# Kernel optimization log

Hardware: AMD Instinct MI355X
Metric: run time of the kernel (lower is better)

Reference implementation:

```python
import jax, jax.numpy as jnp
import numpy as np

NEG = -1e30

def setup_inputs() -> dict:
    key = jax.random.key(0)
    ks = jax.random.split(key, 6)
    B, H, Lc, Lq = 32, 256, 1024, 256
    C = jax.random.normal(ks[0], (B, H, Lc), dtype=jnp.float32)
    Q = jax.random.normal(ks[1], (B, H, Lq), dtype=jnp.float32)
    cmask = jnp.ones((B, Lc), dtype=jnp.int32)
    qmask = jnp.ones((B, Lq), dtype=jnp.int32)
    # xavier_uniform on [3H,1]: bound = sqrt(6/(3H+1))
    bound = float(np.sqrt(6.0 / (3 * H + 1)))
    w = jax.random.uniform(ks[2], (3 * H,), minval=-bound, maxval=bound, dtype=jnp.float32)
    # kaiming_normal (relu, fan_in=4H): std = sqrt(2/(4H))
    W_res = jax.random.normal(ks[3], (H, 4 * H), dtype=jnp.float32) * float(np.sqrt(2.0 / (4 * H)))
    b_res = jnp.zeros((H,), dtype=jnp.float32)
    return {"C": C, "Q": Q, "cmask": cmask, "qmask": qmask, "w": w, "W_res": W_res, "b_res": b_res}

def reference(C, Q, cmask, qmask, w, W_res, b_res):
    H = w.shape[0] // 3
    Ct = jnp.transpose(C, (0, 2, 1))  # [B, Lc, H]
    Qt = jnp.transpose(Q, (0, 2, 1))  # [B, Lq, H]
    w1, w2, w3 = w[:H], w[H:2 * H], w[2 * H:]
    # trilinear similarity S[b,i,j] = Ct_i.w1 + Qt_j.w2 + (Ct_i*Qt_j).w3
    S = (jnp.einsum('blh,h->bl', Ct, w1)[:, :, None]
         + jnp.einsum('bmh,h->bm', Qt, w2)[:, None, :]
         + jnp.einsum('blh,bmh->blm', Ct * w3, Qt))  # [B, Lc, Lq]
    qm = qmask.astype(jnp.float32)[:, None, :]  # [B,1,Lq]
    cm = cmask.astype(jnp.float32)[:, :, None]  # [B,Lc,1]
    S_row = jax.nn.softmax(S + NEG * (1.0 - qm), axis=2)   # over questions
    S_col = jax.nn.softmax(S + NEG * (1.0 - cm), axis=1)   # over context
    A = jnp.einsum('blm,bmh->blh', S_row, Qt)  # [B, Lc, H]
    Bm = jnp.einsum('blm,bkm->blk', S_row, S_col)  # [B, Lc, Lc]
    Bv = jnp.einsum('blk,bkh->blh', Bm, Ct)  # [B, Lc, H]
    cat = jnp.concatenate([Ct, A, Ct * A, Ct * Bv], axis=2)  # [B, Lc, 4H]
    out = jax.nn.relu(jnp.einsum('blf,hf->blh', cat, W_res) + b_res)
    return jnp.transpose(out, (0, 2, 1))  # [B, H, Lc]
```

## Files before the change

### kernel.cpp

```cpp
#include <hip/hip_runtime.h>
#include <math.h>

#define NB 32
#define NH 256
#define NLC 1024
#define NLQ 256
#define NEGV (-1e30f)
#define TCH 8
#define KSPLIT 4

typedef short short8 __attribute__((ext_vector_type(8)));
typedef float f32x4 __attribute__((ext_vector_type(4)));

__device__ inline short bf16_of(float f) {
  union { float f; unsigned u; } v;
  v.f = f;
  unsigned r = (v.u + 0x7fffu + ((v.u >> 16) & 1u)) >> 16;
  return (short)r;
}
__device__ inline float f_of(short s) {
  union { unsigned u; float f; } v;
  v.u = ((unsigned)(unsigned short)s) << 16;
  return v.f;
}
__device__ inline short8 cvt8(float4 a, float4 b) {
  short8 o;
  o[0] = bf16_of(a.x); o[1] = bf16_of(a.y); o[2] = bf16_of(a.z); o[3] = bf16_of(a.w);
  o[4] = bf16_of(b.x); o[5] = bf16_of(b.y); o[6] = bf16_of(b.z); o[7] = bf16_of(b.w);
  return o;
}

#define XCD_SWZ(GX, GY, GZ, bx, by, bz)                                 \
  int bx, by, bz;                                                       \
  {                                                                     \
    int _lin = blockIdx.x + (GX) * (blockIdx.y + (GY) * blockIdx.z);    \
    const int _nwg = (GX) * (GY) * (GZ);                                \
    _lin = (_lin & 7) * (_nwg >> 3) + (_lin >> 3);                      \
    bx = _lin % (GX);                                                   \
    by = (_lin / (GX)) % (GY);                                          \
    bz = _lin / ((GX) * (GY));                                          \
  }

__device__ inline void lds_w8(short* lds, int r, int c, short8 v) {
  int byteoff = (r << 6) + (((c ^ ((r >> 1) & 3)) & 3) << 4);
  *(short8*)((char*)lds + byteoff) = v;
}
__device__ inline short8 lds_r8(const short* lds, int R, int g) {
  int byteoff = (R << 6) + (((g ^ ((R >> 1) & 3)) & 3) << 4);
  return *(const short8*)((const char*)lds + byteoff);
}
__device__ inline void stage_g(const short* src, int ld, short* lds, int t) {
  int L = t & 63, w = t >> 6;
  int cp = (L & 3) ^ ((L >> 3) & 3);
#pragma unroll
  for (int i = 0; i < 2; ++i) {
    int seg = w + i * 4;
    const short* g = src + (size_t)(seg * 16 + (L >> 2)) * ld + cp * 8;
    __builtin_amdgcn_global_load_lds(
        (const __attribute__((address_space(1))) unsigned int*)g,
        (__attribute__((address_space(3))) unsigned int*)(lds + seg * 512), 16,
        0, 0);
  }
}

#define GEMM_IDS                                       \
  int t = threadIdx.x, lane = t & 63, w = t >> 6;      \
  int ln = lane & 15, g = lane >> 4;                   \
  int wr = (w >> 1) << 6, wc = (w & 1) << 6;           \
  (void)wr; (void)wc;

#define MFMA_STEP(AS, BS)                                                      \
  {                                                                            \
    short8 af[4], bfr[4];                                                      \
    _Pragma("unroll") for (int mi = 0; mi < 4; ++mi) af[mi] =                  \
        lds_r8(AS, wr + mi * 16 + ln, g);                                      \
    _Pragma("unroll") for (int ni = 0; ni < 4; ++ni) bfr[ni] =                 \
        lds_r8(BS, wc + ni * 16 + ln, g);                                      \
    _Pragma("unroll") for (int mi = 0; mi < 4; ++mi)                           \
        _Pragma("unroll") for (int ni = 0; ni < 4; ++ni) acc[mi][ni] =         \
            __builtin_amdgcn_mfma_f32_16x16x32_bf16(af[mi], bfr[ni],           \
                                                    acc[mi][ni], 0, 0, 0);     \
  }

__global__ __launch_bounds__(256) void k_prep_c(const float* __restrict__ C,
                                                const float* __restrict__ w,
                                                short* __restrict__ Ct_lh,
                                                short* __restrict__ Cb_hl,
                                                float* __restrict__ s1p) {
  __shared__ float Ts[64][65];
  __shared__ float red[4][64];
  int b = blockIdx.z, h0 = blockIdx.y << 6, l0 = blockIdx.x << 6;
  int t = threadIdx.x;
  int hr = t >> 4, lc = (t & 15) << 2;
  const float* Cb = C + ((size_t)b * NH + h0) * NLC + l0;
#pragma unroll
  for (int i = 0; i < 4; ++i) {
    int h = hr + i * 16;
    float4 v = *(const float4*)&Cb[(size_t)h * NLC + lc];
    short4 cb;
    cb.x = bf16_of(v.x); cb.y = bf16_of(v.y);
    cb.z = bf16_of(v.z); cb.w = bf16_of(v.w);
    *(short4*)&Cb_hl[((size_t)b * NH + h0 + h) * NLC + l0 + lc] = cb;
    Ts[h][lc + 0] = v.x;
    Ts[h][lc + 1] = v.y;
    Ts[h][lc + 2] = v.z;
    Ts[h][lc + 3] = v.w;
  }
  __syncthreads();
  int lr = t >> 2, hc = (t & 3) << 4;
  short* dst = &Ct_lh[((size_t)b * NLC + l0 + lr) * NH + h0 + hc];
  short8 o0, o1;
#pragma unroll
  for (int j = 0; j < 8; ++j) o0[j] = bf16_of(Ts[hc + j][lr]);
#pragma unroll
  for (int j = 0; j < 8; ++j) o1[j] = bf16_of(Ts[hc + 8 + j][lr]);
  *(short8*)dst = o0;
  *(short8*)(dst + 8) = o1;
  int q = t >> 6, lq = t & 63;
  float a = 0.f;
#pragma unroll
  for (int j = 0; j < 16; ++j) a += Ts[(q << 4) + j][lq] * w[h0 + (q << 4) + j];
  red[q][lq] = a;
  __syncthreads();
  if (q == 0)
    s1p[((size_t)blockIdx.y * NB + b) * NLC + l0 + lq] =
        red[0][lq] + red[1][lq] + red[2][lq] + red[3][lq];
}

__global__ __launch_bounds__(256) void k_prep_q(const float* __restrict__ Q,
                                                const float* __restrict__ w,
                                                short* __restrict__ Qtw3,
                                                short* __restrict__ Qb_hm,
                                                float* __restrict__ s2p) {
  __shared__ float Ts[64][65];
  __shared__ float red[4][64];
  int b = blockIdx.z, h0 = blockIdx.y << 6, m0 = blockIdx.x << 6;
  int t = threadIdx.x;
  int hr = t >> 4, mc = (t & 15) << 2;
  const float* w3 = w + 2 * NH;
  const float* Qb = Q + ((size_t)b * NH + h0) * NLQ + m0;
#pragma unroll
  for (int i = 0; i < 4; ++i) {
    int h = hr + i * 16;
    float4 v = *(const float4*)&Qb[(size_t)h * NLQ + mc];
    short4 qb;
    qb.x = bf16_of(v.x); qb.y = bf16_of(v.y);
    qb.z = bf16_of(v.z); qb.w = bf16_of(v.w);
    *(short4*)&Qb_hm[((size_t)b * NH + h0 + h) * NLQ + m0 + mc] = qb;
    Ts[h][mc + 0] = v.x;
    Ts[h][mc + 1] = v.y;
    Ts[h][mc + 2] = v.z;
    Ts[h][mc + 3] = v.w;
  }
  __syncthreads();
  int mr = t >> 2, hc = (t & 3) << 4;
  short* dst = &Qtw3[((size_t)b * NLQ + m0 + mr) * NH + h0 + hc];
  short8 o0, o1;
#pragma unroll
  for (int j = 0; j < 8; ++j)
    o0[j] = bf16_of(Ts[hc + j][mr] * w3[h0 + hc + j]);
#pragma unroll
  for (int j = 0; j < 8; ++j)
    o1[j] = bf16_of(Ts[hc + 8 + j][mr] * w3[h0 + hc + 8 + j]);
  *(short8*)dst = o0;
  *(short8*)(dst + 8) = o1;
  int q = t >> 6, mq = t & 63;
  const float* w2 = w + NH;
  float a = 0.f;
#pragma unroll
  for (int j = 0; j < 16; ++j)
    a += Ts[(q << 4) + j][mq] * w2[h0 + (q << 4) + j];
  red[q][mq] = a;
  __syncthreads();
  if (q == 0)
    s2p[((size_t)blockIdx.y * NB + b) * NLQ + m0 + mq] =
        red[0][mq] + red[1][mq] + red[2][mq] + red[3][mq];
}

__global__ __launch_bounds__(256) void k_prep_bf16(const float* __restrict__ X,
                                                   short* __restrict__ Y) {
  size_t i = ((size_t)blockIdx.x * 256 + threadIdx.x) * 8;
  float4 v0 = *(const float4*)&X[i];
  float4 v1 = *(const float4*)&X[i + 4];
  *(short8*)&Y[i] = cvt8(v0, v1);
}

__global__ __launch_bounds__(256) void k_sgemm(
    const short* __restrict__ Ct_lh, const short* __restrict__ Qtw3,
    const float* __restrict__ s1p, const float* __restrict__ s2p,
    const int* __restrict__ cmask, float* __restrict__ S,
    float* __restrict__ pmax, float* __restrict__ psum) {
  __shared__ short As[2][4096], Bs[2][4096];
  __shared__ float cmsh[128];
  __shared__ float sredm[4][4][16], sreds[4][4][16];
  XCD_SWZ(NLQ / 128, NLC / 128, NB, bx, by, bz)
  int b = bz, l0 = by << 7, m0 = bx << 7;
  GEMM_IDS
  const short* Ag = Ct_lh + ((size_t)b * NLC + l0) * NH;
  const short* Bg = Qtw3 + ((size_t)b * NLQ + m0) * NH;
  f32x4 acc[4][4] = {};
  stage_g(Ag, NH, As[0], t);
  stage_g(Bg, NH, Bs[0], t);
  __syncthreads();
  int cur = 0;
  for (int kn = 32; kn <= NH; kn += 32) {
    if (kn < NH) {
      stage_g(Ag + kn, NH, As[cur ^ 1], t);
      stage_g(Bg + kn, NH, Bs[cur ^ 1], t);
    }
    MFMA_STEP(As[cur], Bs[cur])
    __syncthreads();
    cur ^= 1;
  }
  if (t < 128) cmsh[t] = cmask[b * NLC + l0 + t] ? 0.f : NEGV;
  __syncthreads();
  const int N1 = NB * NLC, N2 = NB * NLQ;
  float s1r[16], ncr[16];
#pragma unroll
  for (int mi = 0; mi < 4; ++mi)
#pragma unroll
    for (int r = 0; r < 4; ++r) {
      int lloc = wr + mi * 16 + g * 4 + r;
      int gl = b * NLC + l0 + lloc;
      s1r[mi * 4 + r] =
          s1p[gl] + s1p[N1 + gl] + s1p[2 * N1 + gl] + s1p[3 * N1 + gl];
      ncr[mi * 4 + r] = cmsh[lloc];
    }
  float s2v[4], mxc[4], smc[4];
#pragma unroll
  for (int ni = 0; ni < 4; ++ni) {
    int gm = b * NLQ + m0 + wc + ni * 16 + ln;
    s2v[ni] = s2p[gm] + s2p[N2 + gm] + s2p[2 * N2 + gm] + s2p[3 * N2 + gm];
    mxc[ni] = -INFINITY;
    smc[ni] = 0.f;
  }
#pragma unroll
  for (int ni = 0; ni < 4; ++ni)
#pragma unroll
    for (int mi = 0; mi < 4; ++mi)
#pragma unroll
      for (int r = 0; r < 4; ++r)
        mxc[ni] = fmaxf(mxc[ni],
                        acc[mi][ni][r] + s1r[mi * 4 + r] + s2v[ni] +
                            ncr[mi * 4 + r]);
#pragma unroll
  for (int ni = 0; ni < 4; ++ni) {
    int m = m0 + wc + ni * 16 + ln;
#pragma unroll
    for (int mi = 0; mi < 4; ++mi)
#pragma unroll
      for (int r = 0; r < 4; ++r) {
        int l = l0 + wr + mi * 16 + g * 4 + r;
        float sv = acc[mi][ni][r] + s1r[mi * 4 + r] + s2v[ni];
        S[((size_t)b * NLC + l) * NLQ + m] = sv;
        smc[ni] += expf(sv + ncr[mi * 4 + r] - mxc[ni]);
      }
  }
#pragma unroll
  for (int off = 16; off <= 32; off <<= 1)
#pragma unroll
    for (int ni = 0; ni < 4; ++ni) {
      float m2 = __shfl_xor(mxc[ni], off);
      float s2x = __shfl_xor(smc[ni], off);
      float nm = fmaxf(mxc[ni], m2);
      smc[ni] = smc[ni] * expf(mxc[ni] - nm) + s2x * expf(m2 - nm);
      mxc[ni] = nm;
    }
  if (lane < 16) {
#pragma unroll
    for (int ni = 0; ni < 4; ++ni) {
      sredm[w][ni][lane] = mxc[ni];
      sreds[w][ni][lane] = smc[ni];
    }
  }
  __syncthreads();
  if (t < 128) {
    int wcsel = t >> 6, nii = (t >> 4) & 3, lnn = t & 15;
    float mA = sredm[wcsel][nii][lnn], sA = sreds[wcsel][nii][lnn];
    float mB = sredm[wcsel + 2][nii][lnn], sB = sreds[wcsel + 2][nii][lnn];
    float nm = fmaxf(mA, mB);
    float sm = sA * expf(mA - nm) + sB * expf(mB - nm);
    int m = m0 + (wcsel << 6) + nii * 16 + lnn;
    size_t base = ((size_t)b * NLQ + m) * TCH + by;
    pmax[base] = nm;
    psum[base] = sm;
  }
}

__global__ __launch_bounds__(256) void k_colfin(const float* __restrict__ pmax,
                                                const float* __restrict__ psum,
                                                float* __restrict__ cmax,
                                                float* __restrict__ cinv) {
  int m = blockIdx.x * 256 + threadIdx.x;
  const float* pm = pmax + (size_t)m * TCH;
  const float* ps = psum + (size_t)m * TCH;
  float mx = pm[0], sm = ps[0];
#pragma unroll
  for (int c = 1; c < TCH; ++c) {
    float m2 = pm[c], s2 = ps[c];
    float nm = fmaxf(mx, m2);
    sm = sm * expf(mx - nm) + s2 * expf(m2 - nm);
    mx = nm;
  }
  cmax[m] = mx;
  cinv[m] = 1.0f / sm;
}

__global__ __launch_bounds__(256) void k_rowsoft(float* __restrict__ S,
                                                 const int* __restrict__ qmask,
                                                 const int* __restrict__ cmask,
                                                 const float* __restrict__ cmax,
                                                 const float* __restrict__ cinv) {
  int wave = threadIdx.x >> 6, lane = threadIdx.x & 63;
  int idx = (blockIdx.x << 2) + wave;
  int b = idx >> 10;
  float* row = S + (size_t)idx * NLQ;
  const int* qm = qmask + b * NLQ;
  int m4 = lane << 2;
  float4 v = *(const float4*)&row[m4];
  int4 q = *(const int4*)&qm[m4];
  float x0 = v.x + (q.x ? 0.f : NEGV);
  float x1 = v.y + (q.y ? 0.f : NEGV);
  float x2 = v.z + (q.z ? 0.f : NEGV);
  float x3 = v.w + (q.w ? 0.f : NEGV);
  float mx = fmaxf(fmaxf(x0, x1), fmaxf(x2, x3));
#pragma unroll
  for (int off = 32; off > 0; off >>= 1) mx = fmaxf(mx, __shfl_xor(mx, off));
  float p0 = expf(x0 - mx), p1 = expf(x1 - mx);
  float p2 = expf(x2 - mx), p3 = expf(x3 - mx);
  float sm = p0 + p1 + p2 + p3;
#pragma unroll
  for (int off = 32; off > 0; off >>= 1) sm += __shfl_xor(sm, off);
  float iv = 1.0f / sm;
  short4 o;
  o.x = bf16_of(p0 * iv);
  o.y = bf16_of(p1 * iv);
  o.z = bf16_of(p2 * iv);
  o.w = bf16_of(p3 * iv);
  float cmf = (float)cmask[idx];
  float4 cm4 = *(const float4*)&cmax[(b << 8) + m4];
  float4 ci4 = *(const float4*)&cinv[(b << 8) + m4];
  short4 oc;
  oc.x = bf16_of(expf(v.x - cm4.x) * ci4.x * cmf);
  oc.y = bf16_of(expf(v.y - cm4.y) * ci4.y * cmf);
  oc.z = bf16_of(expf(v.z - cm4.z) * ci4.z * cmf);
  oc.w = bf16_of(expf(v.w - cm4.w) * ci4.w * cmf);
  *(short4*)((short*)row + m4) = o;
  *(short4*)((short*)row + 256 + m4) = oc;
}

__global__ __launch_bounds__(256) void k_tgemm(const short* __restrict__ Cb_hl,
                                               const short* __restrict__ PcolS,
                                               float* __restrict__ Tp) {
  __shared__ short As[4096], Bs[4096];
  XCD_SWZ(4, KSPLIT, NB, bx, by, bz)
  int b = bz;
  int ks = by;
  int h0 = (bx & 1) << 7;
  int m0 = (bx >> 1) << 7;
  GEMM_IDS
  const short* Ag = Cb_hl + ((size_t)b * NH + h0) * NLC;
  const short* Pb = PcolS + (size_t)b * NLC * 512 + 256 + m0;
  f32x4 acc[4][4] = {};
  int kbeg = ks * (NLC / KSPLIT), kend = kbeg + NLC / KSPLIT;
  int lloc = t >> 3, g2 = lloc >> 3, kin = lloc & 7;
  int mbase = (t & 7) << 4;
  for (int k0 = kbeg; k0 < kend; k0 += 32) {
    __syncthreads();
    stage_g(Ag + k0, NLC, As, t);
    {
      const short* srow = Pb + (size_t)(k0 + lloc) * 512;
      short8 x0 = *(const short8*)&srow[mbase];
      short8 x1 = *(const short8*)&srow[mbase + 8];
#pragma unroll
      for (int j = 0; j < 8; ++j) {
        int R = mbase + j;
        int byteoff =
            (R << 6) + (((g2 ^ ((R >> 1) & 3)) & 3) << 4) + (kin << 1);
        *(short*)((char*)Bs + byteoff) = x0[j];
      }
#pragma unroll
      for (int j = 0; j < 8; ++j) {
        int R = mbase + 8 + j;
        int byteoff =
            (R << 6) + (((g2 ^ ((R >> 1) & 3)) & 3) << 4) + (kin << 1);
        *(short*)((char*)Bs + byteoff) = x1[j];
      }
    }
    __syncthreads();
    MFMA_STEP(As, Bs)
  }
  float* dst = Tp + ((size_t)ks * NB + b) * NH * NLQ;
#pragma unroll
  for (int mi = 0; mi < 4; ++mi)
#pragma unroll
    for (int ni = 0; ni < 4; ++ni)
#pragma unroll
      for (int r = 0; r < 4; ++r) {
        int h = h0 + wr + mi * 16 + g * 4 + r;
        int m = m0 + wc + ni * 16 + ln;
        dst[(size_t)h * NLQ + m] = acc[mi][ni][r];
      }
}

__global__ __launch_bounds__(256) void k_tfin(const float* __restrict__ Tp,
                                              short* __restrict__ Tt) {
  size_t i = ((size_t)blockIdx.x * 256 + threadIdx.x) * 4;
  const size_t stride = (size_t)NB * NH * NLQ;
  float4 s = *(const float4*)&Tp[i];
#pragma unroll
  for (int ks = 1; ks < KSPLIT; ++ks) {
    float4 v = *(const float4*)&Tp[i + ks * stride];
    s.x += v.x; s.y += v.y; s.z += v.z; s.w += v.w;
  }
  short4 o;
  o.x = bf16_of(s.x);
  o.y = bf16_of(s.y);
  o.z = bf16_of(s.z);
  o.w = bf16_of(s.w);
  *(short4*)&Tt[i] = o;
}

__global__ __launch_bounds__(256) void k_abgemm(
    const short* __restrict__ Prow, const short* __restrict__ Qb_hm,
    const short* __restrict__ Tt, const short* __restrict__ Ct_lh,
    short* __restrict__ A_lh, short* __restrict__ CtA_lh,
    short* __restrict__ CtBv_lh) {
  __shared__ short As[2][4096], Bs[2][4096];
  XCD_SWZ(4, NLC / 128, NB, bx, by, bz)
  int b = bz, l0 = by << 7, nb = bx;
  GEMM_IDS
  const short* Ag = Prow + ((size_t)b * NLC + l0) * 512;
  const short* Bbase = (nb < 2)
                           ? Qb_hm + ((size_t)b * NH + nb * 128) * NLQ
                           : Tt + ((size_t)b * NH + (nb - 2) * 128) * NLQ;
  f32x4 acc[4][4] = {};
  stage_g(Ag, 512, As[0], t);
  stage_g(Bbase, NLQ, Bs[0], t);
  __syncthreads();
  int cur = 0;
  for (int kn = 32; kn <= NLQ; kn += 32) {
    if (kn < NLQ) {
      stage_g(Ag + kn, 512, As[cur ^ 1], t);
      stage_g(Bbase + kn, NLQ, Bs[cur ^ 1], t);
    }
    MFMA_STEP(As[cur], Bs[cur])
    __syncthreads();
    cur ^= 1;
  }
  int hbase = (nb & 1) << 7;
  if (nb < 2) {
#pragma unroll
    for (int mi = 0; mi < 4; ++mi)
#pragma unroll
      for (int ni = 0; ni < 4; ++ni)
#pragma unroll
        for (int r = 0; r < 4; ++r) {
          int l = l0 + wr + mi * 16 + g * 4 + r;
          int h = hbase + wc + ni * 16 + ln;
          size_t off = ((size_t)b * NLC + l) * NH + h;
          float a = acc[mi][ni][r];
          A_lh[off] = bf16_of(a);
          CtA_lh[off] = bf16_of(f_of(Ct_lh[off]) * a);
        }
  } else {
#pragma unroll
    for (int mi = 0; mi < 4; ++mi)
#pragma unroll
      for (int ni = 0; ni < 4; ++ni)
#pragma unroll
        for (int r = 0; r < 4; ++r) {
          int l = l0 + wr + mi * 16 + g * 4 + r;
          int h = hbase + wc + ni * 16 + ln;
          size_t off = ((size_t)b * NLC + l) * NH + h;
          CtBv_lh[off] = bf16_of(f_of(Ct_lh[off]) * acc[mi][ni][r]);
        }
  }
}

__global__ __launch_bounds__(256) void k_out(
    const short* __restrict__ Wb, const short* __restrict__ Ct_lh,
    const short* __restrict__ A_lh, const short* __restrict__ CtA_lh,
    const short* __restrict__ CtBv_lh, const float* __restrict__ br,
    float* __restrict__ out) {
  __shared__ short As[2][4096], Bs[2][4096];
  XCD_SWZ(NLC / 128, NH / 128, NB, bx, by, bz)
  int b = bz, h0 = by << 7, l0 = bx << 7;
  GEMM_IDS
  const short* Wg = Wb + (size_t)h0 * (4 * NH);
  size_t boff = ((size_t)b * NLC + l0) * NH;
  f32x4 acc[4][4] = {};
  stage_g(Wg, 4 * NH, As[0], t);
  stage_g(Ct_lh + boff, NH, Bs[0], t);
  __syncthreads();
  int cur = 0;
  for (int kn = 32; kn <= 4 * NH; kn += 32) {
    bool has = kn < 4 * NH;
    if (has) {
      stage_g(Wg + kn, 4 * NH, As[cur ^ 1], t);
      int regn = kn >> 8, kon = kn & 255;
      const short* base = (regn == 0) ? Ct_lh
                          : (regn == 1) ? A_lh
                          : (regn == 2) ? CtA_lh : CtBv_lh;
      stage_g(base + boff + kon, NH, Bs[cur ^ 1], t);
    }
    MFMA_STEP(As[cur], Bs[cur])
    __syncthreads();
    cur ^= 1;
  }
#pragma unroll
  for (int mi = 0; mi < 4; ++mi)
#pragma unroll
    for (int ni = 0; ni < 4; ++ni) {
      int h = h0 + wr + mi * 16 + g * 4;
      int l = l0 + wc + ni * 16 + ln;
#pragma unroll
      for (int r = 0; r < 4; ++r) {
        float bias = br[h + r];
        out[((size_t)b * NH + h + r) * NLC + l] =
            fmaxf(acc[mi][ni][r] + bias, 0.f);
      }
    }
}

extern "C" void kernel_launch(void* const* d_in, const int* in_sizes, int n_in,
                              void* d_out, int out_size, void* d_ws,
                              size_t ws_size, hipStream_t stream) {
  (void)in_sizes;
  (void)n_in;
  (void)out_size;
  (void)ws_size;
  const float* C = (const float*)d_in[0];
  const float* Q = (const float*)d_in[1];
  const int* cmask = (const int*)d_in[2];
  const int* qmask = (const int*)d_in[3];
  const float* w = (const float*)d_in[4];
  const float* W = (const float*)d_in[5];
  const float* br = (const float*)d_in[6];
  float* out = (float*)d_out;

  char* p = (char*)d_ws;
  float* S = (float*)p;       p += (size_t)NB * NLC * NLQ * 4;
  short* Ct_lh = (short*)p;   p += (size_t)NB * NLC * NH * 2;
  short* A_lh = (short*)p;    p += (size_t)NB * NLC * NH * 2;
  short* CtBv_lh = (short*)p; p += (size_t)NB * NLC * NH * 2;
  short* CtA_lh = (short*)p;  p += (size_t)NB * NLC * NH * 2;
  short* Cb_hl = (short*)p;   p += (size_t)NB * NH * NLC * 2;
  short* Tt = (short*)p;      p += (size_t)NB * NH * NLQ * 2;
  short* Qtw3 = (short*)p;    p += (size_t)NB * NLQ * NH * 2;
  short* Qb_hm = (short*)p;   p += (size_t)NB * NH * NLQ * 2;
  short* Wb = (short*)p;      p += (size_t)NH * 4 * NH * 2;
  float* cmax = (float*)p;    p += (size_t)NB * NLQ * 4;
  float* cinv = (float*)p;    p += (size_t)NB * NLQ * 4;
  float* pmax = (float*)p;    p += (size_t)NB * NLQ * TCH * 4;
  float* psum = (float*)p;    p += (size_t)NB * NLQ * TCH * 4;
  float* s1p = (float*)p;     p += (size_t)4 * NB * NLC * 4;
  float* s2p = (float*)p;     p += (size_t)4 * NB * NLQ * 4;
  float* Tp = (float*)A_lh;
  short* Prow = (short*)S;

  k_prep_c<<<dim3(NLC / 64, NH / 64, NB), dim3(256), 0, stream>>>(C, w, Ct_lh,
                                                                  Cb_hl, s1p);
  k_prep_q<<<dim3(NLQ / 64, NH / 64, NB), dim3(256), 0, stream>>>(
      Q, w, Qtw3, Qb_hm, s2p);
  k_prep_bf16<<<dim3(NH * 4 * NH / 2048), dim3(256), 0, stream>>>(W, Wb);
  k_sgemm<<<dim3(NLQ / 128, NLC / 128, NB), dim3(256), 0, stream>>>(
      Ct_lh, Qtw3, s1p, s2p, cmask, S, pmax, psum);
  k_colfin<<<dim3(NB * NLQ / 256), dim3(256), 0, stream>>>(pmax, psum, cmax,
                                                           cinv);
  k_rowsoft<<<dim3(NB * NLC / 4), dim3(256), 0, stream>>>(S, qmask, cmask,
                                                          cmax, cinv);
  k_tgemm<<<dim3(4, KSPLIT, NB), dim3(256), 0, stream>>>(Cb_hl, Prow, Tp);
  k_tfin<<<dim3(NB * NH * NLQ / 1024), dim3(256), 0, stream>>>(Tp, Tt);
  k_abgemm<<<dim3(4, NLC / 128, NB), dim3(256), 0, stream>>>(
      Prow, Qb_hm, Tt, Ct_lh, A_lh, CtA_lh, CtBv_lh);
  k_out<<<dim3(NLC / 128, NH / 128, NB), dim3(256), 0, stream>>>(
      Wb, Ct_lh, A_lh, CtA_lh, CtBv_lh, br, out);
}
```

Before: 139.2 us.

## Store split-K partials in bf16 and retile output GEMM to full-H by 64-row tiles

The split-K partial sums of the T GEMM are now written as bf16 instead of fp32, which halves the traffic through the partial buffer, and the reduce kernel handles 8 elements per thread. The output GEMM now gives each block all 256 output channels and 64 context positions, so every activation tile is read once rather than once per h-half, while W is streamed in two 128-row halves. The cost is extra rounding in the partials and fewer, larger blocks with a bigger LDS footprint for W.

Measured after the change: 140.1 us. Within noise of the previous version (+0.7%).

```diff
diff --git a/kernel.cpp b/kernel.cpp
--- a/kernel.cpp
+++ b/kernel.cpp
@@ -61,6 +61,15 @@
         (__attribute__((address_space(3))) unsigned int*)(lds + seg * 512), 16,
         0, 0);
   }
+}
+__device__ inline void stage_g64(const short* src, int ld, short* lds, int t) {
+  int L = t & 63, w = t >> 6;
+  int cp = (L & 3) ^ ((L >> 3) & 3);
+  const short* g = src + (size_t)(w * 16 + (L >> 2)) * ld + cp * 8;
+  __builtin_amdgcn_global_load_lds(
+      (const __attribute__((address_space(1))) unsigned int*)g,
+      (__attribute__((address_space(3))) unsigned int*)(lds + w * 512), 16, 0,
+      0);
 }
 
 #define GEMM_IDS                                       \
@@ -351,7 +360,7 @@
 
 __global__ __launch_bounds__(256) void k_tgemm(const short* __restrict__ Cb_hl,
                                                const short* __restrict__ PcolS,
-                                               float* __restrict__ Tp) {
+                                               short* __restrict__ Tpb) {
   __shared__ short As[4096], Bs[4096];
   XCD_SWZ(4, KSPLIT, NB, bx, by, bz)
   int b = bz;
@@ -390,7 +399,7 @@
     __syncthreads();
     MFMA_STEP(As, Bs)
   }
-  float* dst = Tp + ((size_t)ks * NB + b) * NH * NLQ;
+  short* dst = Tpb + ((size_t)ks * NB + b) * NH * NLQ;
 #pragma unroll
   for (int mi = 0; mi < 4; ++mi)
 #pragma unroll
@@ -399,26 +408,23 @@
       for (int r = 0; r < 4; ++r) {
         int h = h0 + wr + mi * 16 + g * 4 + r;
         int m = m0 + wc + ni * 16 + ln;
-        dst[(size_t)h * NLQ + m] = acc[mi][ni][r];
+        dst[(size_t)h * NLQ + m] = bf16_of(acc[mi][ni][r]);
       }
 }
 
-__global__ __launch_bounds__(256) void k_tfin(const float* __restrict__ Tp,
+__global__ __launch_bounds__(256) void k_tfin(const short* __restrict__ Tpb,
                                               short* __restrict__ Tt) {
-  size_t i = ((size_t)blockIdx.x * 256 + threadIdx.x) * 4;
+  size_t i = ((size_t)blockIdx.x * 256 + threadIdx.x) * 8;
   const size_t stride = (size_t)NB * NH * NLQ;
-  float4 s = *(const float4*)&Tp[i];
-#pragma unroll
-  for (int ks = 1; ks < KSPLIT; ++ks) {
-    float4 v = *(const float4*)&Tp[i + ks * stride];
-    s.x += v.x; s.y += v.y; s.z += v.z; s.w += v.w;
-  }
-  short4 o;
-  o.x = bf16_of(s.x);
-  o.y = bf16_of(s.y);
-  o.z = bf16_of(s.z);
-  o.w = bf16_of(s.w);
-  *(short4*)&Tt[i] = o;
+  short8 x0 = *(const short8*)&Tpb[i];
+  short8 x1 = *(const short8*)&Tpb[i + stride];
+  short8 x2 = *(const short8*)&Tpb[i + 2 * stride];
+  short8 x3 = *(const short8*)&Tpb[i + 3 * stride];
+  short8 o;
+#pragma unroll
+  for (int j = 0; j < 8; ++j)
+    o[j] = bf16_of(f_of(x0[j]) + f_of(x1[j]) + f_of(x2[j]) + f_of(x3[j]));
+  *(short8*)&Tt[i] = o;
 }
 
 __global__ __launch_bounds__(256) void k_abgemm(
@@ -483,28 +489,44 @@
     const short* __restrict__ A_lh, const short* __restrict__ CtA_lh,
     const short* __restrict__ CtBv_lh, const float* __restrict__ br,
     float* __restrict__ out) {
-  __shared__ short As[2][4096], Bs[2][4096];
-  XCD_SWZ(NLC / 128, NH / 128, NB, bx, by, bz)
-  int b = bz, h0 = by << 7, l0 = bx << 7;
-  GEMM_IDS
-  const short* Wg = Wb + (size_t)h0 * (4 * NH);
+  __shared__ short As[2][8192], Bs[2][2048];
+  XCD_SWZ(NLC / 64, 1, NB, bx, by, bz)
+  int b = bz, l0 = bx << 6;
+  int t = threadIdx.x, lane = t & 63, w = t >> 6;
+  int ln = lane & 15, g = lane >> 4;
   size_t boff = ((size_t)b * NLC + l0) * NH;
   f32x4 acc[4][4] = {};
-  stage_g(Wg, 4 * NH, As[0], t);
-  stage_g(Ct_lh + boff, NH, Bs[0], t);
+  stage_g(Wb, 4 * NH, As[0], t);
+  stage_g(Wb + (size_t)128 * (4 * NH), 4 * NH, As[0] + 4096, t);
+  stage_g64(Ct_lh + boff, NH, Bs[0], t);
   __syncthreads();
   int cur = 0;
   for (int kn = 32; kn <= 4 * NH; kn += 32) {
     bool has = kn < 4 * NH;
     if (has) {
-      stage_g(Wg + kn, 4 * NH, As[cur ^ 1], t);
+      stage_g(Wb + kn, 4 * NH, As[cur ^ 1], t);
+      stage_g(Wb + (size_t)128 * (4 * NH) + kn, 4 * NH, As[cur ^ 1] + 4096, t);
       int regn = kn >> 8, kon = kn & 255;
       const short* base = (regn == 0) ? Ct_lh
                           : (regn == 1) ? A_lh
                           : (regn == 2) ? CtA_lh : CtBv_lh;
-      stage_g(base + boff + kon, NH, Bs[cur ^ 1], t);
-    }
-    MFMA_STEP(As[cur], Bs[cur])
+      stage_g64(base + boff + kon, NH, Bs[cur ^ 1], t);
+    }
+    {
+      short8 af[4], bfr[4];
+#pragma unroll
+      for (int mi = 0; mi < 4; ++mi)
+        af[mi] = lds_r8(As[cur], w * 64 + mi * 16 + ln, g);
+#pragma unroll
+      for (int ni = 0; ni < 4; ++ni)
+        bfr[ni] = lds_r8(Bs[cur], ni * 16 + ln, g);
+#pragma unroll
+      for (int mi = 0; mi < 4; ++mi)
+#pragma unroll
+        for (int ni = 0; ni < 4; ++ni)
+          acc[mi][ni] = __builtin_amdgcn_mfma_f32_16x16x32_bf16(
+              af[mi], bfr[ni], acc[mi][ni], 0, 0, 0);
+    }
     __syncthreads();
     cur ^= 1;
   }
@@ -512,8 +534,8 @@
   for (int mi = 0; mi < 4; ++mi)
 #pragma unroll
     for (int ni = 0; ni < 4; ++ni) {
-      int h = h0 + wr + mi * 16 + g * 4;
-      int l = l0 + wc + ni * 16 + ln;
+      int h = w * 64 + mi * 16 + g * 4;
+      int l = l0 + ni * 16 + ln;
 #pragma unroll
       for (int r = 0; r < 4; ++r) {
         float bias = br[h + r];
@@ -556,7 +578,7 @@
   float* psum = (float*)p;    p += (size_t)NB * NLQ * TCH * 4;
   float* s1p = (float*)p;     p += (size_t)4 * NB * NLC * 4;
   float* s2p = (float*)p;     p += (size_t)4 * NB * NLQ * 4;
-  float* Tp = (float*)A_lh;
+  short* Tpb = A_lh;
   short* Prow = (short*)S;
 
   k_prep_c<<<dim3(NLC / 64, NH / 64, NB), dim3(256), 0, stream>>>(C, w, Ct_lh,
@@ -570,10 +592,10 @@
                                                            cinv);
   k_rowsoft<<<dim3(NB * NLC / 4), dim3(256), 0, stream>>>(S, qmask, cmask,
                                                           cmax, cinv);
-  k_tgemm<<<dim3(4, KSPLIT, NB), dim3(256), 0, stream>>>(Cb_hl, Prow, Tp);
-  k_tfin<<<dim3(NB * NH * NLQ / 1024), dim3(256), 0, stream>>>(Tp, Tt);
+  k_tgemm<<<dim3(4, KSPLIT, NB), dim3(256), 0, stream>>>(Cb_hl, Prow, Tpb);
+  k_tfin<<<dim3(NB * NH * NLQ / 2048), dim3(256), 0, stream>>>(Tpb, Tt);
   k_abgemm<<<dim3(4, NLC / 128, NB), dim3(256), 0, stream>>>(
       Prow, Qb_hm, Tt, Ct_lh, A_lh, CtA_lh, CtBv_lh);
-  k_out<<<dim3(NLC / 128, NH / 128, NB), dim3(256), 0, stream>>>(
+  k_out<<<dim3(NLC / 64, 1, NB), dim3(256), 0, stream>>>(
       Wb, Ct_lh, A_lh, CtA_lh, CtBv_lh, br, out);
 }
```
